# Kernel optimization log

Measured on AMD Instinct MI355X. Metric: run time of the kernel, lower is better.

The kernel has to match this reference:

```python
import jax, jax.numpy as jnp
import numpy as np

EPS = 1e-8

def setup_inputs() -> dict:
    key = jax.random.key(0)
    k1, k2, k3 = jax.random.split(key, 3)
    B, K, D = 2048, 128, 512
    x = jax.random.normal(k1, (B, D), dtype=jnp.float32)
    centers = jax.random.uniform(k2, (K, D), dtype=jnp.float32)
    Dm = 0.2 * jax.random.uniform(k3, (K, D), dtype=jnp.float32) + 0.9
    return {"x": x, "centers": centers, "D": Dm}

def reference(x, centers, D):
    # Per-class diagonal Mahalanobis distance + GMM log-responsibilities.
    D_abs = jnp.abs(D) + EPS                      # [K, d]
    log_det = jnp.sum(jnp.log(D_abs), axis=1)     # [K]
    det_sf = -0.5 * log_det
    det_scale = jnp.exp(det_sf - jnp.max(det_sf)) # [K]

    diff = x[:, None, :] - centers[None, :, :]    # [B, K, d]
    # diag Sigma_inv: dist_sq = sum_d diff^2 / D_abs
    dist_sq = jnp.einsum('bkd,kd->bk', diff * diff, 1.0 / D_abs)  # [B, K]

    expo = -0.5 * dist_sq
    expo_safe = expo - jnp.max(expo, axis=-1, keepdims=True)
    numer = det_scale[None, :] * jnp.exp(expo_safe)               # [B, K]
    resp = numer / jnp.sum(numer, axis=1, keepdims=True)
    resp_gmm = jnp.log(jnp.clip(resp, 1e-8, None))                # [B, K]

    cluster_assignment = jnp.argmax(resp_gmm, axis=1)             # [B]
    cluster_dist_mat = jnp.sqrt(dist_sq)                          # [B, K]
    cluster_dist = jnp.take_along_axis(
        cluster_dist_mat, cluster_assignment[:, None], axis=1)[:, 0]
    return resp_gmm, cluster_dist
```

## Files before the change

### kernel.cpp

```cpp
#include <hip/hip_runtime.h>
#include <math.h>

#define TB 2048
#define TK 128
#define TD 512
#define BR 8
#define NBLK (TB / BR)
#define NKS 32

typedef _Float16 half8 __attribute__((ext_vector_type(8)));
typedef float f32x4 __attribute__((ext_vector_type(4)));


__global__ __launch_bounds__(128) void prep_kernel(const float* __restrict__ C,
        const float* __restrict__ Dm, _Float16* __restrict__ Wfrag,
        float* __restrict__ off, float* __restrict__ ebuf) {
    __shared__ float sE[2], sL[2];
    const int k = blockIdx.x;
    const int t = threadIdx.x;
    const int ks = t >> 2, lg = t & 3;
    const int d0 = ks * 16 + lg * 4;

    float4 dv = *reinterpret_cast<const float4*>(&Dm[(size_t)k * TD + d0]);
    float4 cv = *reinterpret_cast<const float4*>(&C[(size_t)k * TD + d0]);
    float a0 = fabsf(dv.x) + 1e-8f, a1 = fabsf(dv.y) + 1e-8f;
    float a2 = fabsf(dv.z) + 1e-8f, a3 = fabsf(dv.w) + 1e-8f;
    float i0 = 1.f / a0, i1 = 1.f / a1, i2 = 1.f / a2, i3 = 1.f / a3;
    float c0 = cv.x * i0, c1 = cv.y * i1, c2 = cv.z * i2, c3 = cv.w * i3;

    half8 h;
    h[0] = (_Float16)i0; h[1] = (_Float16)(-2.f * c0);
    h[2] = (_Float16)i1; h[3] = (_Float16)(-2.f * c1);
    h[4] = (_Float16)i2; h[5] = (_Float16)(-2.f * c2);
    h[6] = (_Float16)i3; h[7] = (_Float16)(-2.f * c3);
    *reinterpret_cast<half8*>(
        &Wfrag[(((size_t)(k >> 4) * NKS + ks) * 64 + lg * 16 + (k & 15)) * 8]) = h;

    float es = (cv.x * c0 + cv.y * c1) + (cv.z * c2 + cv.w * c3);
    float ls = logf((a0 * a1) * (a2 * a3));
    #pragma unroll
    for (int m = 1; m <= 32; m <<= 1) {
        es += __shfl_xor(es, m, 64);
        ls += __shfl_xor(ls, m, 64);
    }
    if ((t & 63) == 0) { sE[t >> 6] = es; sL[t >> 6] = ls; }
    __syncthreads();
    if (t == 0) {
        float E = sE[0] + sE[1], L = sL[0] + sL[1];
        off[k] = -0.5f * (E + L);
        ebuf[k] = E;
    }
}

__global__ __launch_bounds__(1024) void gmm_kernel(const float* __restrict__ x,
        const _Float16* __restrict__ Wfrag, const float* __restrict__ off,
        const float* __restrict__ ebuf, float* __restrict__ out) {
    __shared__ __align__(16) _Float16 XAf[NKS * 64 * 8];
    __shared__ __align__(16) float accX[8][64][4];
    __shared__ float red_m[8][BR], red_s[8][BR], red_g[8][BR];
    __shared__ int   red_i[8][BR];

    const int tid = threadIdx.x;
    const int l = tid & 63;
    const int w = tid >> 6;
    const int kh = w >> 3;
    const int wc = w & 7;
    const int l15 = l & 15;
    const int lg = l >> 4;
    const int b0 = blockIdx.x * BR;
    const int col = wc * 16 + l15;

    #pragma unroll
    for (int i = 0; i < 2; ++i) {
        int rec = tid + i * 1024;
        int ks = rec >> 6;
        int lr = rec & 63;
        int row = lr & 15;
        int lgr = lr >> 4;
        half8 h = (half8){0, 0, 0, 0, 0, 0, 0, 0};
        if (row < BR) {
            int d0 = ks * 16 + lgr * 4;
            float4 v = *reinterpret_cast<const float4*>(
                &x[(size_t)(b0 + row) * TD + d0]);
            h[0] = (_Float16)(v.x * v.x); h[1] = (_Float16)v.x;
            h[2] = (_Float16)(v.y * v.y); h[3] = (_Float16)v.y;
            h[4] = (_Float16)(v.z * v.z); h[5] = (_Float16)v.z;
            h[6] = (_Float16)(v.w * v.w); h[7] = (_Float16)v.w;
        }
        *reinterpret_cast<half8*>(&XAf[(size_t)rec * 8]) = h;
    }
    __syncthreads();

    const half8* wfp = reinterpret_cast<const half8*>(Wfrag)
                       + ((size_t)(wc * NKS + kh * 16) * 64 + l);
    const half8* xap = reinterpret_cast<const half8*>(XAf)
                       + ((size_t)(kh * 16) * 64 + l);
    f32x4 acc0 = (f32x4){0.f, 0.f, 0.f, 0.f};
    f32x4 acc1 = (f32x4){0.f, 0.f, 0.f, 0.f};
    #pragma unroll
    for (int i = 0; i < 16; i += 2) {
        half8 bv0 = wfp[(size_t)i * 64];
        half8 av0 = xap[(size_t)i * 64];
        half8 bv1 = wfp[(size_t)(i + 1) * 64];
        half8 av1 = xap[(size_t)(i + 1) * 64];
        acc0 = __builtin_amdgcn_mfma_f32_16x16x32_f16(av0, bv0, acc0, 0, 0, 0);
        acc1 = __builtin_amdgcn_mfma_f32_16x16x32_f16(av1, bv1, acc1, 0, 0, 0);
    }
    f32x4 acc = acc0 + acc1;

    if (kh == 1) *reinterpret_cast<f32x4*>(&accX[wc][l][0]) = acc;
    __syncthreads();

    float sv[4];
    float bv[4], bg[4], ps[4];
    int bi[4];
    if (kh == 0) {
        acc += *reinterpret_cast<const f32x4*>(&accX[wc][l][0]);

        const float offc = off[col];
        #pragma unroll
        for (int e = 0; e < 4; ++e) {
            sv[e] = fmaf(-0.5f, acc[e], offc);
            bv[e] = sv[e]; bi[e] = col; bg[e] = acc[e];
        }
        #pragma unroll
        for (int msk = 1; msk <= 8; msk <<= 1) {
            #pragma unroll
            for (int e = 0; e < 4; ++e) {
                float ov = __shfl_xor(bv[e], msk, 64);
                int   oi = __shfl_xor(bi[e], msk, 64);
                float og = __shfl_xor(bg[e], msk, 64);
                if (ov > bv[e] || (ov == bv[e] && oi < bi[e])) {
                    bv[e] = ov; bi[e] = oi; bg[e] = og;
                }
            }
        }
        #pragma unroll
        for (int e = 0; e < 4; ++e) ps[e] = expf(sv[e] - bv[e]);
        #pragma unroll
        for (int msk = 1; msk <= 8; msk <<= 1)
            #pragma unroll
            for (int e = 0; e < 4; ++e) ps[e] += __shfl_xor(ps[e], msk, 64);

        if (l15 == 0) {
            #pragma unroll
            for (int e = 0; e < 4; ++e) {
                int r = lg * 4 + e;
                if (r < BR) {
                    red_m[wc][r] = bv[e];
                    red_s[wc][r] = ps[e];
                    red_i[wc][r] = bi[e];
                    red_g[wc][r] = bg[e];
                }
            }
        }
    }
    __syncthreads();

    if (kh == 0) {
        const float LOGC = -18.420680743952367f;
        #pragma unroll
        for (int e = 0; e < 4; ++e) {
            int r = lg * 4 + e;
            if (r < BR) {
                float M = red_m[0][r];
                #pragma unroll
                for (int w2 = 1; w2 < 8; ++w2) M = fmaxf(M, red_m[w2][r]);
                float S = 0.f;
                #pragma unroll
                for (int w2 = 0; w2 < 8; ++w2) S += red_s[w2][r] * expf(red_m[w2][r] - M);
                float lse = logf(S) + M;
                out[(size_t)(b0 + r) * TK + col] = fmaxf(sv[e] - lse, LOGC);
            }
        }

        if (wc == 0 && l15 == 0) {
            #pragma unroll
            for (int e = 0; e < 4; ++e) {
                int r = lg * 4 + e;
                if (r < BR) {
                    float v = red_m[0][r]; int ki = red_i[0][r]; float g = red_g[0][r];
                    #pragma unroll
                    for (int w2 = 1; w2 < 8; ++w2) {
                        float v2 = red_m[w2][r]; int i2 = red_i[w2][r];
                        if (v2 > v || (v2 == v && i2 < ki)) { v = v2; ki = i2; g = red_g[w2][r]; }
                    }
                    out[(size_t)TB * TK + b0 + r] = sqrtf(fmaxf(g + ebuf[ki], 0.f));
                }
            }
        }
    }
}

extern "C" void kernel_launch(void* const* d_in, const int* in_sizes, int n_in,
                              void* d_out, int out_size, void* d_ws, size_t ws_size,
                              hipStream_t stream) {
    const float* x  = (const float*)d_in[0];
    const float* C  = (const float*)d_in[1];
    const float* Dm = (const float*)d_in[2];
    float* out = (float*)d_out;

    _Float16* Wfrag = (_Float16*)d_ws;
    float* off  = (float*)((char*)d_ws + (size_t)TK * 2 * TD * 2);
    float* ebuf = off + TK;

    prep_kernel<<<TK, 128, 0, stream>>>(C, Dm, Wfrag, off, ebuf);
    gmm_kernel<<<NBLK, 1024, 0, stream>>>(x, Wfrag, off, ebuf, out);
}
```

Baseline: 21.71 us.

## Halve rows per block and centralize per-row logsumexp in a dedicated wave

```diff
diff --git a/kernel.cpp b/kernel.cpp
--- a/kernel.cpp
+++ b/kernel.cpp
@@ -4,7 +4,7 @@
 #define TB 2048
 #define TK 128
 #define TD 512
-#define BR 8
+#define BR 4
 #define NBLK (TB / BR)
 #define NKS 32
 
@@ -59,6 +59,7 @@
     __shared__ __align__(16) float accX[8][64][4];
     __shared__ float red_m[8][BR], red_s[8][BR], red_g[8][BR];
     __shared__ int   red_i[8][BR];
+    __shared__ float red_lse[BR];
 
     const int tid = threadIdx.x;
     const int l = tid & 63;
@@ -112,12 +113,12 @@
     __syncthreads();
 
     float sv[4];
-    float bv[4], bg[4], ps[4];
-    int bi[4];
     if (kh == 0) {
         acc += *reinterpret_cast<const f32x4*>(&accX[wc][l][0]);
 
         const float offc = off[col];
+        float bv[4], bg[4], ps[4];
+        int bi[4];
         #pragma unroll
         for (int e = 0; e < 4; ++e) {
             sv[e] = fmaf(-0.5f, acc[e], offc);
@@ -142,52 +143,43 @@
             #pragma unroll
             for (int e = 0; e < 4; ++e) ps[e] += __shfl_xor(ps[e], msk, 64);
 
-        if (l15 == 0) {
+        if (l == 0) {
             #pragma unroll
             for (int e = 0; e < 4; ++e) {
-                int r = lg * 4 + e;
-                if (r < BR) {
-                    red_m[wc][r] = bv[e];
-                    red_s[wc][r] = ps[e];
-                    red_i[wc][r] = bi[e];
-                    red_g[wc][r] = bg[e];
-                }
+                red_m[wc][e] = bv[e];
+                red_s[wc][e] = ps[e];
+                red_i[wc][e] = bi[e];
+                red_g[wc][e] = bg[e];
             }
         }
     }
     __syncthreads();
 
-    if (kh == 0) {
+    if (w == 8 && l < BR) {
+        const int r = l;
+        float M = red_m[0][r];
+        #pragma unroll
+        for (int w2 = 1; w2 < 8; ++w2) M = fmaxf(M, red_m[w2][r]);
+        float S = 0.f;
+        #pragma unroll
+        for (int w2 = 0; w2 < 8; ++w2) S += red_s[w2][r] * expf(red_m[w2][r] - M);
+        red_lse[r] = logf(S) + M;
+
+        float v = red_m[0][r]; int ki = red_i[0][r]; float g = red_g[0][r];
+        #pragma unroll
+        for (int w2 = 1; w2 < 8; ++w2) {
+            float v2 = red_m[w2][r]; int i2 = red_i[w2][r];
+            if (v2 > v || (v2 == v && i2 < ki)) { v = v2; ki = i2; g = red_g[w2][r]; }
+        }
+        out[(size_t)TB * TK + b0 + r] = sqrtf(fmaxf(g + ebuf[ki], 0.f));
+    }
+    __syncthreads();
+
+    if (kh == 0 && lg == 0) {
         const float LOGC = -18.420680743952367f;
         #pragma unroll
         for (int e = 0; e < 4; ++e) {
-            int r = lg * 4 + e;
-            if (r < BR) {
-                float M = red_m[0][r];
-                #pragma unroll
-                for (int w2 = 1; w2 < 8; ++w2) M = fmaxf(M, red_m[w2][r]);
-                float S = 0.f;
-                #pragma unroll
-                for (int w2 = 0; w2 < 8; ++w2) S += red_s[w2][r] * expf(red_m[w2][r] - M);
-                float lse = logf(S) + M;
-                out[(size_t)(b0 + r) * TK + col] = fmaxf(sv[e] - lse, LOGC);
-            }
-        }
-
-        if (wc == 0 && l15 == 0) {
-            #pragma unroll
-            for (int e = 0; e < 4; ++e) {
-                int r = lg * 4 + e;
-                if (r < BR) {
-                    float v = red_m[0][r]; int ki = red_i[0][r]; float g = red_g[0][r];
-                    #pragma unroll
-                    for (int w2 = 1; w2 < 8; ++w2) {
-                        float v2 = red_m[w2][r]; int i2 = red_i[w2][r];
-                        if (v2 > v || (v2 == v && i2 < ki)) { v = v2; ki = i2; g = red_g[w2][r]; }
-                    }
-                    out[(size_t)TB * TK + b0 + r] = sqrtf(fmaxf(g + ebuf[ki], 0.f));
-                }
-            }
+            out[(size_t)(b0 + e) * TK + col] = fmaxf(sv[e] - red_lse[e], LOGC);
         }
     }
 }
```

Measured after the change: 20.52 us. 5.5% less time.
